# Kernel optimization log

Measured on AMD Instinct MI355X. Metric: run time of the kernel, lower is better.

## Reference

```python
import jax, jax.numpy as jnp
import numpy as np

N_NODES = 100000
N_EDGES = 1600000
IN_DIM = 128
HID = 64


def setup_inputs() -> dict:
    key = jax.random.key(0)
    ks = jax.random.split(key, 12)
    s = 1.0 / np.sqrt(IN_DIM)
    sh = 1.0 / np.sqrt(HID)
    return {
        "x": jax.random.normal(ks[0], (N_NODES, IN_DIM), jnp.float32),
        "edge_index": jax.random.randint(ks[1], (2, N_EDGES), 0, N_NODES, jnp.int64)
        if jax.config.jax_enable_x64 else jax.random.randint(ks[1], (2, N_EDGES), 0, N_NODES, jnp.int32),
        "edge_attr": jax.random.uniform(ks[2], (N_EDGES, 1), jnp.float32),
        "Wi": jax.random.normal(ks[3], (IN_DIM, HID), jnp.float32) * s,
        "bi": jnp.zeros((HID,), jnp.float32),
        "W1": jax.random.normal(ks[4], (HID, HID), jnp.float32) * sh,
        "b1": jnp.zeros((HID,), jnp.float32),
        "W2": jax.random.normal(ks[5], (HID, HID), jnp.float32) * sh,
        "b2": jnp.zeros((HID,), jnp.float32),
        "W3": jax.random.normal(ks[6], (HID, HID), jnp.float32) * sh,
        "b3": jnp.zeros((HID,), jnp.float32),
    }


def reference(x, edge_index, edge_attr, Wi, bi, W1, b1, W2, b2, W3, b3):
    src = edge_index[0]
    tgt = edge_index[1]
    w = edge_attr[:, 0:1]  # [E,1]
    h = jax.nn.relu(x @ Wi + bi)  # [N,H]
    states = [h]
    for W, b in ((W1, b1), (W2, b2), (W3, b3)):
        # per-edge weighted message, scatter-add into target nodes
        msgs = jax.ops.segment_sum(h[src] * w, tgt, num_segments=h.shape[0])
        h = jax.nn.relu((h + msgs) @ W + b)
        states.append(h)
    return jnp.stack(states)  # [4, N, H] (list of states in the original)
```

## Files before the change

kernel.cpp:

```cpp
#include <hip/hip_runtime.h>
#include <hip/hip_bf16.h>

#define N_NODES 100000
#define N_EDGES 1600000
#define IN_DIM  128
#define HID     64
#define CAP_N   64
#define CNT_STRIDE 16

#define SC_EB   1024
#define SC_BLOCKS ((N_EDGES + SC_EB - 1) / SC_EB)
#define GEMM_BLOCKS ((N_NODES + 63) / 64)

#define PITCH_IN  152
#define PITCH_HID 88

typedef __attribute__((ext_vector_type(8))) short bf16x8;
typedef __attribute__((ext_vector_type(4))) float f32x4;

__device__ inline unsigned short f2bf(float f) {
    __hip_bfloat16 b = __float2bfloat16(f);
    return *reinterpret_cast<unsigned short*>(&b);
}

__global__ void wf_prep_kernel(const float* __restrict__ Wi,
                               const float* __restrict__ W1,
                               const float* __restrict__ W2,
                               const float* __restrict__ W3,
                               unsigned short* __restrict__ wf_in,
                               unsigned short* __restrict__ wf_hid,
                               int* __restrict__ cnt) {
    int t = blockIdx.x * 256 + threadIdx.x;
    if (t < N_NODES) cnt[(size_t)t * CNT_STRIDE] = 0;
    if (t < 8192) {
        int j = t & 7, n16 = (t >> 3) & 15, quad = (t >> 7) & 3, nt = (t >> 9) & 3, kc = t >> 11;
        int k = kc * 32 + quad * 8 + j, n = nt * 16 + n16;
        wf_in[t] = f2bf(Wi[k * HID + n]);
    }
    if (t < 4096) {
        int j = t & 7, n16 = (t >> 3) & 15, quad = (t >> 7) & 3, nt = (t >> 9) & 3, kc = t >> 11;
        int k = kc * 32 + quad * 8 + j, n = nt * 16 + n16;
        wf_hid[t]        = f2bf(W1[k * HID + n]);
        wf_hid[4096 + t] = f2bf(W2[k * HID + n]);
        wf_hid[8192 + t] = f2bf(W3[k * HID + n]);
    }
}

__global__ __launch_bounds__(256) void fused_scatter_gemm_kernel(
        const int* __restrict__ src,
        const int* __restrict__ tgt,
        const float* __restrict__ ea,
        int* __restrict__ cnt,
        int2* __restrict__ binned,
        const float* __restrict__ x,
        const unsigned short* __restrict__ wf,
        const float* __restrict__ bi,
        float* __restrict__ h0,
        __hip_bfloat16* __restrict__ hbf) {
    __shared__ unsigned short sX[64 * PITCH_IN];
    const int tid = threadIdx.x;

    if ((blockIdx.x & 1) == 0) {
        const int s  = blockIdx.x >> 1;
        const int e0 = s * SC_EB;
        #pragma unroll
        for (int k = 0; k < SC_EB / 256; ++k) {
            int e = e0 + tid + k * 256;
            if (e < N_EDGES) {
                int t = tgt[e];
                int r = atomicAdd(&cnt[(size_t)t * CNT_STRIDE], 1);
                if (r < CAP_N)
                    binned[(size_t)t * CAP_N + r] =
                        make_int2(src[e], __float_as_int(ea[e]));
            }
        }
        return;
    }

    const int row0 = (blockIdx.x >> 1) * 64;

    #pragma unroll
    for (int it = 0; it < 8; ++it) {
        int i  = tid + it * 256;
        int r  = i >> 5;
        int kq = i & 31;
        int rg = row0 + r;
        float4 v = (rg < N_NODES)
                 ? ((const float4*)x)[(size_t)rg * (IN_DIM / 4) + kq]
                 : make_float4(0.f, 0.f, 0.f, 0.f);
        ushort4 pk;
        pk.x = f2bf(v.x); pk.y = f2bf(v.y); pk.z = f2bf(v.z); pk.w = f2bf(v.w);
        *(ushort4*)(sX + r * PITCH_IN + kq * 4) = pk;
    }
    __syncthreads();

    const int lane = tid & 63;
    const int wid  = tid >> 6;
    const int l16  = lane & 15;
    const int q    = lane >> 4;

    f32x4 acc[4] = {{0,0,0,0},{0,0,0,0},{0,0,0,0},{0,0,0,0}};
    const bf16x8* wf8 = (const bf16x8*)wf;

    #pragma unroll
    for (int kc = 0; kc < 4; ++kc) {
        bf16x8 af = *(const bf16x8*)(sX + (wid * 16 + l16) * PITCH_IN + kc * 32 + q * 8);
        #pragma unroll
        for (int nt = 0; nt < 4; ++nt) {
            bf16x8 bfr = wf8[((kc * 4 + nt) * 4 + q) * 16 + l16];
            acc[nt] = __builtin_amdgcn_mfma_f32_16x16x32_bf16(af, bfr, acc[nt], 0, 0, 0);
        }
    }

    #pragma unroll
    for (int nt = 0; nt < 4; ++nt) {
        float bb = bi[nt * 16 + l16];
        #pragma unroll
        for (int reg = 0; reg < 4; ++reg) {
            int rg = row0 + wid * 16 + q * 4 + reg;
            if (rg < N_NODES) {
                float v = fmaxf(acc[nt][reg] + bb, 0.0f);
                h0 [(size_t)rg * HID + nt * 16 + l16] = v;
                hbf[(size_t)rg * HID + nt * 16 + l16] = __float2bfloat16(v);
            }
        }
    }
}

__global__ __launch_bounds__(256) void agg_gemm_kernel(
        const float* __restrict__ h,
        const __hip_bfloat16* __restrict__ hbf_in,
        const int* __restrict__ cnt,
        const int2* __restrict__ binned,
        const unsigned short* __restrict__ wf,
        const float* __restrict__ b,
        float* __restrict__ hnext,
        __hip_bfloat16* __restrict__ hbf_out,
        const int store_bf) {
    __shared__ unsigned short sXs[64 * PITCH_HID];
    const int tid  = threadIdx.x;
    const int row0 = blockIdx.x * 64;
    const int lane = tid & 63;
    const int wid  = tid >> 6;
    const int grp  = lane >> 4;
    const int sub  = lane & 15;

    const int node0 = row0 + wid * 16;

    int cv = 0;
    {
        int nl = node0 + (lane & 15);
        if (lane < 16 && nl < N_NODES)
            cv = min(cnt[(size_t)nl * CNT_STRIDE], CAP_N);
    }

    int c0 = __shfl(cv, 0);
    int2 pl = binned[(size_t)min(node0, N_NODES - 1) * CAP_N + min(lane, max(c0 - 1, 0))];

    for (int t = 0; t < 16; ++t) {
        const int node = node0 + t;
        const int ccur = __shfl(cv, t);
        const int2 pl_cur = pl;
        if (t < 15) {
            int cn = __shfl(cv, t + 1);
            pl = binned[(size_t)min(node + 1, N_NODES - 1) * CAP_N
                        + min(lane, max(cn - 1, 0))];
        }
        if (node < N_NODES) {
            float ax = 0.f, ay = 0.f, az = 0.f, aw = 0.f;
            const int last = ccur - 1;
            for (int i = 0; i < ccur; i += 8) {
                int e0 = i + grp;
                int e1 = i + 4 + grp;
                bool l0 = (e0 <= last);
                bool l1 = (e1 <= last);
                int s0  = __shfl(pl_cur.x, l0 ? e0 : last);
                int w0i = __shfl(pl_cur.y, l0 ? e0 : last);
                int s1  = __shfl(pl_cur.x, l1 ? e1 : last);
                int w1i = __shfl(pl_cur.y, l1 ? e1 : last);
                uint2 g0 = *(const uint2*)(hbf_in + (size_t)s0 * HID + sub * 4);
                uint2 g1 = *(const uint2*)(hbf_in + (size_t)s1 * HID + sub * 4);
                float w0 = l0 ? __int_as_float(w0i) : 0.0f;
                float w1 = l1 ? __int_as_float(w1i) : 0.0f;
                ax += w0 * __uint_as_float(g0.x << 16);
                ay += w0 * __uint_as_float(g0.x & 0xFFFF0000u);
                az += w0 * __uint_as_float(g0.y << 16);
                aw += w0 * __uint_as_float(g0.y & 0xFFFF0000u);
                ax += w1 * __uint_as_float(g1.x << 16);
                ay += w1 * __uint_as_float(g1.x & 0xFFFF0000u);
                az += w1 * __uint_as_float(g1.y << 16);
                aw += w1 * __uint_as_float(g1.y & 0xFFFF0000u);
            }
            ax += __shfl_xor(ax, 16); ay += __shfl_xor(ay, 16);
            az += __shfl_xor(az, 16); aw += __shfl_xor(aw, 16);
            ax += __shfl_xor(ax, 32); ay += __shfl_xor(ay, 32);
            az += __shfl_xor(az, 32); aw += __shfl_xor(aw, 32);
            if (grp == 0) {
                const float4 hv = *(const float4*)(h + (size_t)node * HID + sub * 4);
                ushort4 pk;
                pk.x = f2bf(hv.x + ax); pk.y = f2bf(hv.y + ay);
                pk.z = f2bf(hv.z + az); pk.w = f2bf(hv.w + aw);
                *(ushort4*)(sXs + (wid * 16 + t) * PITCH_HID + sub * 4) = pk;
            }
        } else if (grp == 0) {
            ushort4 z; z.x = 0; z.y = 0; z.z = 0; z.w = 0;
            *(ushort4*)(sXs + (wid * 16 + t) * PITCH_HID + sub * 4) = z;
        }
    }
    __syncthreads();

    const int l16 = lane & 15;
    const int q   = lane >> 4;

    f32x4 acc[4] = {{0,0,0,0},{0,0,0,0},{0,0,0,0},{0,0,0,0}};
    const bf16x8* wf8 = (const bf16x8*)wf;

    #pragma unroll
    for (int kc = 0; kc < 2; ++kc) {
        bf16x8 af = *(const bf16x8*)(sXs + (wid * 16 + l16) * PITCH_HID + kc * 32 + q * 8);
        #pragma unroll
        for (int nt = 0; nt < 4; ++nt) {
            bf16x8 bfr = wf8[((kc * 4 + nt) * 4 + q) * 16 + l16];
            acc[nt] = __builtin_amdgcn_mfma_f32_16x16x32_bf16(af, bfr, acc[nt], 0, 0, 0);
        }
    }

    #pragma unroll
    for (int nt = 0; nt < 4; ++nt) {
        float bb = b[nt * 16 + l16];
        #pragma unroll
        for (int reg = 0; reg < 4; ++reg) {
            int rg = row0 + wid * 16 + q * 4 + reg;
            if (rg < N_NODES) {
                float v = fmaxf(acc[nt][reg] + bb, 0.0f);
                hnext[(size_t)rg * HID + nt * 16 + l16] = v;
                if (store_bf)
                    hbf_out[(size_t)rg * HID + nt * 16 + l16] = __float2bfloat16(v);
            }
        }
    }
}

extern "C" void kernel_launch(void* const* d_in, const int* in_sizes, int n_in,
                              void* d_out, int out_size, void* d_ws, size_t ws_size,
                              hipStream_t stream) {
    const float* x   = (const float*)d_in[0];
    const int*   ei  = (const int*)  d_in[1];
    const float* ea  = (const float*)d_in[2];
    const float* Wi  = (const float*)d_in[3];
    const float* bi  = (const float*)d_in[4];
    const float* W1  = (const float*)d_in[5];
    const float* b1  = (const float*)d_in[6];
    const float* W2  = (const float*)d_in[7];
    const float* b2  = (const float*)d_in[8];
    const float* W3  = (const float*)d_in[9];
    const float* b3  = (const float*)d_in[10];
    const float* bl[3] = { b1, b2, b3 };
    float* out = (float*)d_out;

    const int* src = ei;
    const int* tgt = ei + N_EDGES;

    int2* binned = (int2*)d_ws;
    int* cnt = (int*)(binned + (size_t)N_NODES * CAP_N);
    __hip_bfloat16* hbf0 = (__hip_bfloat16*)(cnt + (size_t)N_NODES * CNT_STRIDE);
    __hip_bfloat16* hbf1 = hbf0 + (size_t)N_NODES * HID;
    unsigned short* wf_in  = (unsigned short*)(hbf1 + (size_t)N_NODES * HID);
    unsigned short* wf_hid = wf_in + 8192;

    const int prep_blocks = (N_NODES + 255) / 256;
    wf_prep_kernel<<<prep_blocks, 256, 0, stream>>>(Wi, W1, W2, W3,
                                                    wf_in, wf_hid, cnt);

    fused_scatter_gemm_kernel<<<SC_BLOCKS + GEMM_BLOCKS, 256, 0, stream>>>(
        src, tgt, ea, cnt, binned, x, wf_in, bi, out, hbf0);

    __hip_bfloat16* hin  = hbf0;
    __hip_bfloat16* hout = hbf1;
    for (int l = 0; l < 3; ++l) {
        const float* hl = out + (size_t)l * N_NODES * HID;
        float* hn       = out + (size_t)(l + 1) * N_NODES * HID;
        agg_gemm_kernel<<<GEMM_BLOCKS, 256, 0, stream>>>(
            hl, hin, cnt, binned,
            wf_hid + (size_t)l * 4096, bl[l], hn, hout, (l < 2) ? 1 : 0);
        __hip_bfloat16* t = hin; hin = hout; hout = t;
    }
}
```

Measured before the change: 397.7 us.

## Compact padded per-node edge bins into CSR arrays before aggregation layers

Three new kernels run after the scatter stage: a per-block degree sum, a single-block scan and a compaction pass. Together they turn the padded 64-slot-per-node binned edge lists into a dense CSR layout with offsets, counts and packed (src, weight) pairs. The three aggregation layers then read contiguous pairs instead of padded bins, aiming for better cache-line use and fewer scattered reads of the count array. The cost is three extra launches plus a full pass over the binned data.

```diff
diff --git a/kernel.cpp b/kernel.cpp
--- a/kernel.cpp
+++ b/kernel.cpp
@@ -7,10 +7,12 @@
 #define HID     64
 #define CAP_N   64
 #define CNT_STRIDE 16
+#define PAIRS_LIM (N_EDGES - 1)
 
 #define SC_EB   1024
 #define SC_BLOCKS ((N_EDGES + SC_EB - 1) / SC_EB)
 #define GEMM_BLOCKS ((N_NODES + 63) / 64)
+#define PREP_BLOCKS ((N_NODES + 255) / 256)
 
 #define PITCH_IN  152
 #define PITCH_HID 88
@@ -127,11 +129,81 @@
     }
 }
 
+__global__ __launch_bounds__(256) void csr_partial_kernel(
+        const int* __restrict__ cnt, int* __restrict__ bsum) {
+    __shared__ int s[4];
+    int t = blockIdx.x * 256 + threadIdx.x;
+    int v = (t < N_NODES) ? min(cnt[(size_t)t * CNT_STRIDE], CAP_N) : 0;
+    #pragma unroll
+    for (int d = 1; d < 64; d <<= 1) v += __shfl_xor(v, d);
+    if ((threadIdx.x & 63) == 0) s[threadIdx.x >> 6] = v;
+    __syncthreads();
+    if (threadIdx.x == 0) bsum[blockIdx.x] = s[0] + s[1] + s[2] + s[3];
+}
+
+__global__ void csr_scan_kernel(const int* __restrict__ bsum,
+                                int* __restrict__ boffs) {
+    __shared__ int s[512];
+    const int tid = threadIdx.x;
+    int v = (tid < PREP_BLOCKS) ? bsum[tid] : 0;
+    s[tid] = v;
+    __syncthreads();
+    for (int off = 1; off < 512; off <<= 1) {
+        int t = (tid >= off) ? s[tid - off] : 0;
+        __syncthreads();
+        s[tid] += t;
+        __syncthreads();
+    }
+    if (tid < PREP_BLOCKS) boffs[tid] = s[tid] - v;
+}
+
+__global__ __launch_bounds__(256) void csr_compact_kernel(
+        const int* __restrict__ cnt,
+        const int* __restrict__ boffs,
+        const int2* __restrict__ binned,
+        int* __restrict__ offs,
+        int* __restrict__ counts,
+        int2* __restrict__ pairs) {
+    __shared__ int soff[256], scnt[256];
+    __shared__ int wsum[4];
+    const int b = blockIdx.x, tid = threadIdx.x;
+    const int node = b * 256 + tid;
+    int v = (node < N_NODES) ? min(cnt[(size_t)node * CNT_STRIDE], CAP_N) : 0;
+    const int lane = tid & 63, wid = tid >> 6;
+    int sc = v;
+    #pragma unroll
+    for (int d = 1; d < 64; d <<= 1) {
+        int t = __shfl_up(sc, d);
+        if (lane >= d) sc += t;
+    }
+    if (lane == 63) wsum[wid] = sc;
+    __syncthreads();
+    int wb = 0;
+    for (int w = 0; w < wid; ++w) wb += wsum[w];
+    int excl = boffs[b] + wb + sc - v;
+    soff[tid] = excl;
+    scnt[tid] = v;
+    if (node < N_NODES) { offs[node] = excl; counts[node] = v; }
+    __syncthreads();
+
+    const int g = tid >> 4, sub = tid & 15;
+    for (int j = g; j < 256; j += 16) {
+        int n2 = b * 256 + j;
+        if (n2 < N_NODES) {
+            int c = scnt[j], o = soff[j];
+            const int2* sp = binned + (size_t)n2 * CAP_N;
+            for (int i = sub; i < c; i += 16)
+                pairs[o + i] = sp[i];
+        }
+    }
+}
+
 __global__ __launch_bounds__(256) void agg_gemm_kernel(
         const float* __restrict__ h,
         const __hip_bfloat16* __restrict__ hbf_in,
-        const int* __restrict__ cnt,
-        const int2* __restrict__ binned,
+        const int* __restrict__ offs,
+        const int* __restrict__ counts,
+        const int2* __restrict__ pairs,
         const unsigned short* __restrict__ wf,
         const float* __restrict__ b,
         float* __restrict__ hnext,
@@ -146,25 +218,19 @@
     const int sub  = lane & 15;
 
     const int node0 = row0 + wid * 16;
-
-    int cv = 0;
-    {
-        int nl = node0 + (lane & 15);
-        if (lane < 16 && nl < N_NODES)
-            cv = min(cnt[(size_t)nl * CNT_STRIDE], CAP_N);
-    }
-
-    int c0 = __shfl(cv, 0);
-    int2 pl = binned[(size_t)min(node0, N_NODES - 1) * CAP_N + min(lane, max(c0 - 1, 0))];
+    int beg_n = 0, cnt_n = 0;
+    if (node0 < N_NODES) { beg_n = offs[node0]; cnt_n = counts[node0]; }
+    int2 pl = pairs[min(beg_n + lane, PAIRS_LIM)];
 
     for (int t = 0; t < 16; ++t) {
         const int node = node0 + t;
-        const int ccur = __shfl(cv, t);
+        const int ccur = cnt_n;
         const int2 pl_cur = pl;
         if (t < 15) {
-            int cn = __shfl(cv, t + 1);
-            pl = binned[(size_t)min(node + 1, N_NODES - 1) * CAP_N
-                        + min(lane, max(cn - 1, 0))];
+            int nn = node + 1;
+            if (nn < N_NODES) { beg_n = offs[nn]; cnt_n = counts[nn]; }
+            else              { beg_n = 0;        cnt_n = 0; }
+            pl = pairs[min(beg_n + lane, PAIRS_LIM)];
         }
         if (node < N_NODES) {
             float ax = 0.f, ay = 0.f, az = 0.f, aw = 0.f;
@@ -263,17 +329,26 @@
 
     int2* binned = (int2*)d_ws;
     int* cnt = (int*)(binned + (size_t)N_NODES * CAP_N);
-    __hip_bfloat16* hbf0 = (__hip_bfloat16*)(cnt + (size_t)N_NODES * CNT_STRIDE);
+    int2* pairs = (int2*)(cnt + (size_t)N_NODES * CNT_STRIDE);
+    int* offs   = (int*)(pairs + N_EDGES);
+    int* counts = offs + N_NODES;
+    int* bsum   = counts + N_NODES;
+    int* boffs  = bsum + PREP_BLOCKS;
+    __hip_bfloat16* hbf0 = (__hip_bfloat16*)(boffs + PREP_BLOCKS + 2);
     __hip_bfloat16* hbf1 = hbf0 + (size_t)N_NODES * HID;
     unsigned short* wf_in  = (unsigned short*)(hbf1 + (size_t)N_NODES * HID);
     unsigned short* wf_hid = wf_in + 8192;
 
-    const int prep_blocks = (N_NODES + 255) / 256;
-    wf_prep_kernel<<<prep_blocks, 256, 0, stream>>>(Wi, W1, W2, W3,
+    wf_prep_kernel<<<PREP_BLOCKS, 256, 0, stream>>>(Wi, W1, W2, W3,
                                                     wf_in, wf_hid, cnt);
 
     fused_scatter_gemm_kernel<<<SC_BLOCKS + GEMM_BLOCKS, 256, 0, stream>>>(
         src, tgt, ea, cnt, binned, x, wf_in, bi, out, hbf0);
+
+    csr_partial_kernel<<<PREP_BLOCKS, 256, 0, stream>>>(cnt, bsum);
+    csr_scan_kernel   <<<1, 512, 0, stream>>>(bsum, boffs);
+    csr_compact_kernel<<<PREP_BLOCKS, 256, 0, stream>>>(cnt, boffs, binned,
+                                                        offs, counts, pairs);
 
     __hip_bfloat16* hin  = hbf0;
     __hip_bfloat16* hout = hbf1;
@@ -281,7 +356,7 @@
         const float* hl = out + (size_t)l * N_NODES * HID;
         float* hn       = out + (size_t)(l + 1) * N_NODES * HID;
         agg_gemm_kernel<<<GEMM_BLOCKS, 256, 0, stream>>>(
-            hl, hin, cnt, binned,
+            hl, hin, offs, counts, pairs,
             wf_hid + (size_t)l * 4096, bl[l], hn, hout, (l < 2) ? 1 : 0);
         __hip_bfloat16* t = hin; hin = hout; hout = t;
     }
```

New measurement: 472.1 us. 1.19x slower.
